# Performance work log

Hardware: AMD Instinct MI355X
Metric: run time of the kernel (lower is better)

Reference implementation:

```python
import jax, jax.numpy as jnp
import numpy as np

B, N, D, H, LH, AH = 4, 2048, 512, 4, 64, 64
NUM_BUCKETS = 128
EPS = 1e-6
LENGTHS = np.array([2048, 1536, 1024, 1792])  # jagged per-sequence lengths, sum = 6400


def _ln(x, eps=EPS):
    # F.layer_norm without affine params (biased variance)
    m = jnp.mean(x, axis=-1, keepdims=True)
    v = jnp.var(x, axis=-1, keepdims=True)
    return (x - m) * jax.lax.rsqrt(v + eps)


def _rel_bias(all_timestamps, ts_w):
    # bucketed time-delta relative attention bias -> [B, N, N]
    delta = (all_timestamps[:, :, None] - all_timestamps[:, None, :]).astype(jnp.float32)
    bucket = jnp.clip(jnp.floor(jnp.log1p(jnp.abs(delta))).astype(jnp.int32), 0, NUM_BUCKETS)
    return ts_w[bucket]


def setup_inputs() -> dict:
    key = jax.random.key(0)
    ks = jax.random.split(key, 6)
    offsets = np.concatenate([[0], np.cumsum(LENGTHS)]).astype(np.int32)
    T = int(offsets[-1])
    token_batch = np.repeat(np.arange(B), LENGTHS).astype(np.int32)
    token_pos = np.concatenate([np.arange(l) for l in LENGTHS]).astype(np.int32)
    x = jax.random.normal(ks[0], (T, D), jnp.float32)
    uvqk = jax.random.normal(ks[1], (D, 2 * LH * H + 2 * AH * H), jnp.float32) * 0.02
    o_w = jax.random.normal(ks[2], (D, LH * H), jnp.float32) * 0.02  # torch Linear weight [out, in]
    o_b = jnp.zeros((D,), jnp.float32)
    ts_w = jax.random.normal(ks[3], (NUM_BUCKETS + 1,), jnp.float32) * 0.02
    all_timestamps = jnp.sort(jax.random.randint(ks[4], (B, N), 0, 1000000, jnp.int32), axis=-1)
    invalid_attn_mask = jnp.tril(jnp.ones((N, N), jnp.float32))  # causal validity mask in {0,1}
    return {
        'x': x, 'uvqk': uvqk, 'o_w': o_w, 'o_b': o_b, 'ts_w': ts_w,
        'all_timestamps': all_timestamps, 'invalid_attn_mask': invalid_attn_mask,
        'x_offsets': jnp.asarray(offsets), 'token_batch': jnp.asarray(token_batch),
        'token_pos': jnp.asarray(token_pos),
    }


def reference(x, uvqk, o_w, o_b, ts_w, all_timestamps, invalid_attn_mask,
              x_offsets, token_batch, token_pos):
    # input layernorm + fused uvqk projection with SiLU
    h = jax.nn.silu(_ln(x) @ uvqk)  # [T, 2*H*LH + 2*H*AH]
    u, v, q, k = jnp.split(h, [LH * H, 2 * LH * H, 2 * LH * H + AH * H], axis=1)

    def pad(vals):  # jagged [T, d] -> padded dense [B, N, d]
        return jnp.zeros((B, N, vals.shape[-1]), vals.dtype).at[token_batch, token_pos].set(vals)

    pq = pad(q).reshape(B, N, H, AH)
    pk = pad(k).reshape(B, N, H, AH)
    pv = pad(v).reshape(B, N, H, LH)

    scores = jnp.einsum('bnhd,bmhd->bhnm', pq, pk)
    scores = scores + _rel_bias(all_timestamps, ts_w)[:, None]  # broadcast over heads
    scores = jax.nn.silu(scores) / N
    scores = scores * invalid_attn_mask[None, None]
    attn = jnp.einsum('bhnm,bmhd->bnhd', scores, pv).reshape(B, N, H * LH)
    attn_j = attn[token_batch, token_pos]  # dense -> jagged [T, H*LH]

    o_in = u * _ln(attn_j)
    return o_in @ o_w.T + o_b + x
```

## Files before the change

kernel.cpp:

```cpp
#include <hip/hip_runtime.h>
#include <math.h>


typedef __attribute__((ext_vector_type(8))) short bf16x8;
typedef __attribute__((ext_vector_type(4))) float f32x4;

__device__ __forceinline__ float silu_over_2048(float v) {
    return v * __builtin_amdgcn_rcpf(2048.0f + 2048.0f * __expf(-v));
}

__device__ __forceinline__ float silu_f(float v) {
    return v * __builtin_amdgcn_rcpf(1.0f + __expf(-v));
}

__device__ __forceinline__ unsigned short f2bf(float f) {
    unsigned int u = __float_as_uint(f);
    u += 0x7fffu + ((u >> 16) & 1u);
    return (unsigned short)(u >> 16);
}

__global__ __launch_bounds__(256) void k1_ln_prep(const float* __restrict__ x,
                                                  unsigned short* __restrict__ xnb,
                                                  const float* __restrict__ uvqk,
                                                  unsigned short* __restrict__ uvqkT,
                                                  const float* __restrict__ ow,
                                                  unsigned short* __restrict__ owb) {
    __shared__ float L[64][68];
    const int tid = threadIdx.x;
    const int bx = blockIdx.x;
    if (bx < 6400) {
        const float* xr = x + bx * 512;
        float a = xr[tid];
        float b = xr[tid + 256];
        float s = a + b, ss = a * a + b * b;
#pragma unroll
        for (int off = 32; off > 0; off >>= 1) {
            s += __shfl_down(s, off);
            ss += __shfl_down(ss, off);
        }
        float* red = &L[0][0];
        if ((tid & 63) == 0) { red[tid >> 6] = s; red[4 + (tid >> 6)] = ss; }
        __syncthreads();
        s = red[0] + red[1] + red[2] + red[3];
        ss = red[4] + red[5] + red[6] + red[7];
        const float mean = s * (1.0f / 512.0f);
        const float var = ss * (1.0f / 512.0f) - mean * mean;
        const float rstd = rsqrtf(var + 1e-6f);
        xnb[bx * 512 + tid] = f2bf((a - mean) * rstd);
        xnb[bx * 512 + tid + 256] = f2bf((b - mean) * rstd);
    } else if (bx < 6528) {
        const int t = bx - 6400;
        const int n0 = (t & 15) * 64;
        const int k0 = (t >> 4) * 64;
#pragma unroll
        for (int i = 0; i < 4; ++i) {
            const int r = (tid >> 4) + i * 16;
            const int c = (tid & 15) * 4;
            *(float4*)&L[r][c] = *(const float4*)(uvqk + (k0 + r) * 1024 + n0 + c);
        }
        __syncthreads();
        const int n = tid >> 2;
        const int kb = (tid & 3) * 16;
#pragma unroll
        for (int pass = 0; pass < 2; ++pass) {
            unsigned short pk[8];
#pragma unroll
            for (int j = 0; j < 8; ++j) pk[j] = f2bf(L[kb + pass * 8 + j][n]);
            *(uint4*)(uvqkT + (n0 + n) * 512 + k0 + kb + pass * 8) = *(const uint4*)pk;
        }
    } else {
        const int base = ((bx - 6528) * 256 + tid) * 8;
        float4 a = *(const float4*)(ow + base);
        float4 b = *(const float4*)(ow + base + 4);
        unsigned short pk[8] = {f2bf(a.x), f2bf(a.y), f2bf(a.z), f2bf(a.w),
                                f2bf(b.x), f2bf(b.y), f2bf(b.z), f2bf(b.w)};
        *(uint4*)(owb + base) = *(const uint4*)pk;
    }
}

__global__ __launch_bounds__(256, 4) void k2_gemm1(const unsigned short* __restrict__ A,
                                                   const unsigned short* __restrict__ Bt,
                                                   float* __restrict__ u_out,
                                                   unsigned short* __restrict__ hb,
                                                   unsigned short* __restrict__ vtb) {
    __shared__ __align__(16) unsigned short As[64][72];
    __shared__ __align__(16) unsigned short Bs[64][72];
    const int tid = threadIdx.x;
    const int lane = tid & 63;
    const int w = tid >> 6;
    const int l15 = lane & 15;
    const int quad = lane >> 4;
    const int bm = blockIdx.y * 64;
    const int bn = blockIdx.x * 64;

    f32x4 acc[4] = {};
    for (int kc = 0; kc < 512; kc += 64) {
        __syncthreads();
#pragma unroll
        for (int i = 0; i < 2; ++i) {
            const int r = (tid >> 3) + i * 32;
            const int c = (tid & 7) * 8;
            *(uint4*)&As[r][c] = *(const uint4*)(A + (bm + r) * 512 + kc + c);
            *(uint4*)&Bs[r][c] = *(const uint4*)(Bt + (bn + r) * 512 + kc + c);
        }
        __syncthreads();
        const bf16x8 a0 = *(const bf16x8*)&As[w * 16 + l15][quad * 8];
        const bf16x8 a1 = *(const bf16x8*)&As[w * 16 + l15][32 + quad * 8];
#pragma unroll
        for (int nt = 0; nt < 4; ++nt) {
            bf16x8 b0 = *(const bf16x8*)&Bs[nt * 16 + l15][quad * 8];
            bf16x8 b1 = *(const bf16x8*)&Bs[nt * 16 + l15][32 + quad * 8];
            acc[nt] = __builtin_amdgcn_mfma_f32_16x16x32_bf16(a0, b0, acc[nt], 0, 0, 0);
            acc[nt] = __builtin_amdgcn_mfma_f32_16x16x32_bf16(a1, b1, acc[nt], 0, 0, 0);
        }
    }
    const int m = bm + w * 16 + quad * 4;
    if (bn < 256) {
#pragma unroll
        for (int nt = 0; nt < 4; ++nt)
#pragma unroll
            for (int reg = 0; reg < 4; ++reg)
                u_out[(m + reg) * 256 + bn + nt * 16 + l15] = silu_f(acc[nt][reg]);
    } else if (bn < 512) {
        __syncthreads();
#pragma unroll
        for (int nt = 0; nt < 4; ++nt) {
            unsigned short pk[4];
#pragma unroll
            for (int reg = 0; reg < 4; ++reg) pk[reg] = f2bf(silu_f(acc[nt][reg]));
            *(uint2*)&As[nt * 16 + l15][w * 16 + quad * 4] = *(const uint2*)pk;
        }
        __syncthreads();
        const int sr = tid >> 3, sc = (tid & 7) * 8;
#pragma unroll
        for (int i = 0; i < 2; ++i) {
            const int r = sr + i * 32;
            *(uint4*)(vtb + (size_t)(bn - 256 + r) * 6400 + bm + sc) =
                *(const uint4*)&As[r][sc];
        }
    } else {
#pragma unroll
        for (int nt = 0; nt < 4; ++nt)
#pragma unroll
            for (int reg = 0; reg < 4; ++reg)
                hb[(m + reg) * 768 + (bn - 256) + nt * 16 + l15] = f2bf(silu_f(acc[nt][reg]));
    }
}

__global__ __launch_bounds__(256, 5) void k3_attn(const unsigned short* __restrict__ hb,
                                                  const unsigned short* __restrict__ vtb,
                                                  const int* __restrict__ ts,
                                                  const float* __restrict__ tsw,
                                                  const int* __restrict__ offs,
                                                  float* __restrict__ part) {
    const int qt = 31 - (blockIdx.x & 31);
    const int c = blockIdx.x >> 5;
    const int b = blockIdx.y;
    const int hd = blockIdx.z;
    const int off = offs[b];
    const int len = offs[b + 1] - off;
    const int nqt = len >> 6;
    if (qt >= nqt || c * 4 > qt) return;
    const int q0 = qt * 64;
    const int kt_lo = c * 4;
    const int kt_hi = min(qt, c * 4 + 3);

    __shared__ __align__(16) unsigned short QPs[64][72];
    __shared__ __align__(16) unsigned short Ks[64][72];
    __shared__ __align__(16) unsigned short Vt[64][72];
    __shared__ float tqf[64], tkf[64];
    __shared__ float tw[132];

    const int tid = threadIdx.x;
    const int lane = tid & 63;
    const int w = tid >> 6;
    const int l15 = lane & 15;
    const int quad = lane >> 4;
    const int sr = tid >> 3;
    const int sc = (tid & 7) * 8;

    if (tid < 129) tw[tid] = tsw[tid];
    if (tid < 64) tqf[tid] = (float)ts[b * 2048 + q0 + tid];
#pragma unroll
    for (int i = 0; i < 2; ++i)
        *(uint4*)&QPs[sr + i * 32][sc] =
            *(const uint4*)(hb + (off + q0 + sr + i * 32) * 768 + 256 + hd * 64 + sc);
    __syncthreads();

    const bf16x8 aQ0 = *(const bf16x8*)&QPs[w * 16 + l15][quad * 8];
    const bf16x8 aQ1 = *(const bf16x8*)&QPs[w * 16 + l15][32 + quad * 8];
    const f32x4 tq4 = *(const f32x4*)&tqf[w * 16 + quad * 4];
    const int nbase = q0 + w * 16 + quad * 4;

    f32x4 oacc[4] = {};

    for (int kt = kt_lo; kt <= kt_hi; ++kt) {
        const int m0 = kt * 64;
        __syncthreads();
#pragma unroll
        for (int i = 0; i < 2; ++i) {
            const int r = sr + i * 32;
            *(uint4*)&Ks[r][sc] =
                *(const uint4*)(hb + (off + m0 + r) * 768 + 512 + hd * 64 + sc);
            *(uint4*)&Vt[r][sc] =
                *(const uint4*)(vtb + (size_t)(hd * 64 + r) * 6400 + off + m0 + sc);
        }
        if (tid < 64) tkf[tid] = (float)ts[b * 2048 + m0 + tid];
        __syncthreads();

        f32x4 s[4] = {};
#pragma unroll
        for (int nt = 0; nt < 4; ++nt) {
            bf16x8 b0 = *(const bf16x8*)&Ks[nt * 16 + l15][quad * 8];
            bf16x8 b1 = *(const bf16x8*)&Ks[nt * 16 + l15][32 + quad * 8];
            s[nt] = __builtin_amdgcn_mfma_f32_16x16x32_bf16(aQ0, b0, s[nt], 0, 0, 0);
            s[nt] = __builtin_amdgcn_mfma_f32_16x16x32_bf16(aQ1, b1, s[nt], 0, 0, 0);
        }

        const bool diag = (kt == qt);
#pragma unroll
        for (int nt = 0; nt < 4; ++nt) {
            const int m = m0 + nt * 16 + l15;
            const float tk = tkf[nt * 16 + l15];
#pragma unroll
            for (int reg = 0; reg < 4; ++reg) {
                const float delta = fabsf(tq4[reg] - tk);
                const int bucket = (int)(__log2f(1.0f + delta) * 0.6931471805599453f);
                float val = s[nt][reg] + tw[bucket];
                float p = silu_over_2048(val);
                if (diag) p = (m <= nbase + reg) ? p : 0.0f;
                QPs[w * 16 + quad * 4 + reg][nt * 16 + l15] = f2bf(p);
            }
        }

        const bf16x8 aP0 = *(const bf16x8*)&QPs[w * 16 + l15][quad * 8];
        const bf16x8 aP1 = *(const bf16x8*)&QPs[w * 16 + l15][32 + quad * 8];
#pragma unroll
        for (int nt = 0; nt < 4; ++nt) {
            bf16x8 v0 = *(const bf16x8*)&Vt[nt * 16 + l15][quad * 8];
            bf16x8 v1 = *(const bf16x8*)&Vt[nt * 16 + l15][32 + quad * 8];
            oacc[nt] = __builtin_amdgcn_mfma_f32_16x16x32_bf16(aP0, v0, oacc[nt], 0, 0, 0);
            oacc[nt] = __builtin_amdgcn_mfma_f32_16x16x32_bf16(aP1, v1, oacc[nt], 0, 0, 0);
        }
    }

    float* pc = part + (size_t)c * (6400 * 256);
#pragma unroll
    for (int nt = 0; nt < 4; ++nt)
#pragma unroll
        for (int reg = 0; reg < 4; ++reg)
            pc[(off + q0 + w * 16 + quad * 4 + reg) * 256 + hd * 64 + nt * 16 + l15] =
                oacc[nt][reg];
}

__global__ __launch_bounds__(256) void k4a_ln(const float* __restrict__ part,
                                              const float* __restrict__ u_in,
                                              const int* __restrict__ token_pos,
                                              unsigned short* __restrict__ o_in) {
    const int row = blockIdx.x;
    const int tid = threadIdx.x;
    const int qt = token_pos[row] >> 6;
    const int nch = (qt + 4) >> 2;
    float a = 0.0f;
    for (int c = 0; c < nch; ++c) a += part[(size_t)c * (6400 * 256) + row * 256 + tid];
    float s = a, ss = a * a;
#pragma unroll
    for (int off = 32; off > 0; off >>= 1) {
        s += __shfl_down(s, off);
        ss += __shfl_down(ss, off);
    }
    __shared__ float red[8];
    if ((tid & 63) == 0) { red[tid >> 6] = s; red[4 + (tid >> 6)] = ss; }
    __syncthreads();
    s = red[0] + red[1] + red[2] + red[3];
    ss = red[4] + red[5] + red[6] + red[7];
    const float mean = s * (1.0f / 256.0f);
    const float var = ss * (1.0f / 256.0f) - mean * mean;
    const float rstd = rsqrtf(var + 1e-6f);
    const float u = u_in[row * 256 + tid];
    o_in[row * 256 + tid] = f2bf(u * (a - mean) * rstd);
}

__global__ __launch_bounds__(256, 4) void k4b_gemm2(const unsigned short* __restrict__ A,
                                                    const unsigned short* __restrict__ owb,
                                                    const float* __restrict__ ob,
                                                    const float* __restrict__ x,
                                                    float* __restrict__ out) {
    __shared__ __align__(16) unsigned short As[64][72];
    __shared__ __align__(16) unsigned short Bs[64][72];
    const int tid = threadIdx.x;
    const int lane = tid & 63;
    const int w = tid >> 6;
    const int l15 = lane & 15;
    const int quad = lane >> 4;
    const int bm = blockIdx.y * 64;
    const int bn = blockIdx.x * 64;

    f32x4 acc[4] = {};
    for (int kc = 0; kc < 256; kc += 64) {
        __syncthreads();
#pragma unroll
        for (int i = 0; i < 2; ++i) {
            const int r = (tid >> 3) + i * 32;
            const int c = (tid & 7) * 8;
            *(uint4*)&As[r][c] = *(const uint4*)(A + (bm + r) * 256 + kc + c);
            *(uint4*)&Bs[r][c] = *(const uint4*)(owb + (bn + r) * 256 + kc + c);
        }
        __syncthreads();
        const bf16x8 a0 = *(const bf16x8*)&As[w * 16 + l15][quad * 8];
        const bf16x8 a1 = *(const bf16x8*)&As[w * 16 + l15][32 + quad * 8];
#pragma unroll
        for (int nt = 0; nt < 4; ++nt) {
            bf16x8 b0 = *(const bf16x8*)&Bs[nt * 16 + l15][quad * 8];
            bf16x8 b1 = *(const bf16x8*)&Bs[nt * 16 + l15][32 + quad * 8];
            acc[nt] = __builtin_amdgcn_mfma_f32_16x16x32_bf16(a0, b0, acc[nt], 0, 0, 0);
            acc[nt] = __builtin_amdgcn_mfma_f32_16x16x32_bf16(a1, b1, acc[nt], 0, 0, 0);
        }
    }
    const int m = bm + w * 16 + quad * 4;
#pragma unroll
    for (int nt = 0; nt < 4; ++nt) {
        const int d = bn + nt * 16 + l15;
        const float bias = ob[d];
#pragma unroll
        for (int reg = 0; reg < 4; ++reg)
            out[(m + reg) * 512 + d] = acc[nt][reg] + bias + x[(m + reg) * 512 + d];
    }
}

extern "C" void kernel_launch(void* const* d_in, const int* in_sizes, int n_in,
                              void* d_out, int out_size, void* d_ws, size_t ws_size,
                              hipStream_t stream) {
    const float* x = (const float*)d_in[0];
    const float* uvqk = (const float*)d_in[1];
    const float* ow = (const float*)d_in[2];
    const float* ob = (const float*)d_in[3];
    const float* tsw = (const float*)d_in[4];
    const int* ts = (const int*)d_in[5];
    const int* offs = (const int*)d_in[7];
    const int* token_pos = (const int*)d_in[9];
    float* out = (float*)d_out;

    float* ws = (float*)d_ws;
    float* u = ws;
    float* part = u + 6400 * 256;
    unsigned short* xnb = (unsigned short*)(part + 8 * 6400 * 256);
    unsigned short* hb = xnb + 6400 * 512;
    unsigned short* o_in = hb + 6400 * 768;
    unsigned short* uvqkT = o_in + 6400 * 256;
    unsigned short* owb = uvqkT + 1024 * 512;
    unsigned short* vtb = owb + 512 * 256;

    k1_ln_prep<<<6592, 256, 0, stream>>>(x, xnb, uvqk, uvqkT, ow, owb);
    k2_gemm1<<<dim3(16, 100), 256, 0, stream>>>(xnb, uvqkT, u, hb, vtb);
    k3_attn<<<dim3(256, 4, 4), 256, 0, stream>>>(hb, vtb, ts, tsw, offs, part);
    k4a_ln<<<6400, 256, 0, stream>>>(part, u, token_pos, o_in);
    k4b_gemm2<<<dim3(8, 100), 256, 0, stream>>>(o_in, owb, ob, x, out);
}
```

Baseline: 162.7 us.

## Fuse attention-output layernorm into output projection GEMM

Merges the per-row layernorm kernel (which sums attention partials, normalises and multiplies by u) with the output-projection GEMM. Each block now covers 64 rows and 256 output columns, normalises its rows straight into LDS as bf16, and reads weights directly from global memory. This removes one kernel launch and the bf16 o_in round-trip through global memory. In exchange, the partial-sum layernorm is recomputed by both column blocks, so partial-buffer reads double, and the grid shrinks to 200 blocks, which lowers parallelism.

New measurement: 171.8 us. 1.06x slower.

```diff
diff --git a/kernel.cpp b/kernel.cpp
--- a/kernel.cpp
+++ b/kernel.cpp
@@ -253,78 +253,95 @@
                 oacc[nt][reg];
 }
 
-__global__ __launch_bounds__(256) void k4a_ln(const float* __restrict__ part,
-                                              const float* __restrict__ u_in,
-                                              const int* __restrict__ token_pos,
-                                              unsigned short* __restrict__ o_in) {
-    const int row = blockIdx.x;
+__global__ __launch_bounds__(256, 4) void k4_fused(const float* __restrict__ part,
+                                                   const float* __restrict__ u_in,
+                                                   const int* __restrict__ token_pos,
+                                                   const unsigned short* __restrict__ owb,
+                                                   const float* __restrict__ ob,
+                                                   const float* __restrict__ x,
+                                                   float* __restrict__ out) {
+    __shared__ __align__(16) unsigned short oin[64][264];
     const int tid = threadIdx.x;
-    const int qt = token_pos[row] >> 6;
-    const int nch = (qt + 4) >> 2;
-    float a = 0.0f;
-    for (int c = 0; c < nch; ++c) a += part[(size_t)c * (6400 * 256) + row * 256 + tid];
-    float s = a, ss = a * a;
-#pragma unroll
-    for (int off = 32; off > 0; off >>= 1) {
-        s += __shfl_down(s, off);
-        ss += __shfl_down(ss, off);
-    }
-    __shared__ float red[8];
-    if ((tid & 63) == 0) { red[tid >> 6] = s; red[4 + (tid >> 6)] = ss; }
+    const int bm = blockIdx.y * 64;
+    const int dn0 = blockIdx.x * 256;
+
+    {
+        const int rl = tid >> 2;
+        const int cseg = (tid & 3) * 64;
+        const int qt = token_pos[bm] >> 6;
+        const int nch = (qt + 4) >> 2;
+        f32x4 a[16] = {};
+        for (int c = 0; c < nch; ++c) {
+            const float* pr = part + (size_t)c * (6400 * 256) + (bm + rl) * 256 + cseg;
+#pragma unroll
+            for (int j = 0; j < 16; ++j) {
+                const f32x4 v = *(const f32x4*)(pr + j * 4);
+                a[j] += v;
+            }
+        }
+        float s = 0.0f, ss = 0.0f;
+#pragma unroll
+        for (int j = 0; j < 16; ++j)
+#pragma unroll
+            for (int e = 0; e < 4; ++e) { s += a[j][e]; ss += a[j][e] * a[j][e]; }
+        s += __shfl_xor(s, 1); ss += __shfl_xor(ss, 1);
+        s += __shfl_xor(s, 2); ss += __shfl_xor(ss, 2);
+        const float mean = s * (1.0f / 256.0f);
+        const float var = ss * (1.0f / 256.0f) - mean * mean;
+        const float rstd = rsqrtf(var + 1e-6f);
+        const float* ur = u_in + (bm + rl) * 256 + cseg;
+#pragma unroll
+        for (int j = 0; j < 16; j += 2) {
+            const f32x4 u0 = *(const f32x4*)(ur + j * 4);
+            const f32x4 u1 = *(const f32x4*)(ur + j * 4 + 4);
+            unsigned short pk[8];
+#pragma unroll
+            for (int e = 0; e < 4; ++e) {
+                pk[e] = f2bf(u0[e] * (a[j][e] - mean) * rstd);
+                pk[4 + e] = f2bf(u1[e] * (a[j + 1][e] - mean) * rstd);
+            }
+            *(uint4*)&oin[rl][cseg + j * 4] = *(const uint4*)pk;
+        }
+    }
     __syncthreads();
-    s = red[0] + red[1] + red[2] + red[3];
-    ss = red[4] + red[5] + red[6] + red[7];
-    const float mean = s * (1.0f / 256.0f);
-    const float var = ss * (1.0f / 256.0f) - mean * mean;
-    const float rstd = rsqrtf(var + 1e-6f);
-    const float u = u_in[row * 256 + tid];
-    o_in[row * 256 + tid] = f2bf(u * (a - mean) * rstd);
-}
-
-__global__ __launch_bounds__(256, 4) void k4b_gemm2(const unsigned short* __restrict__ A,
-                                                    const unsigned short* __restrict__ owb,
-                                                    const float* __restrict__ ob,
-                                                    const float* __restrict__ x,
-                                                    float* __restrict__ out) {
-    __shared__ __align__(16) unsigned short As[64][72];
-    __shared__ __align__(16) unsigned short Bs[64][72];
-    const int tid = threadIdx.x;
+
     const int lane = tid & 63;
     const int w = tid >> 6;
     const int l15 = lane & 15;
     const int quad = lane >> 4;
-    const int bm = blockIdx.y * 64;
-    const int bn = blockIdx.x * 64;
-
-    f32x4 acc[4] = {};
+    const int dw = dn0 + w * 64;
+
+    f32x4 acc[4][4] = {};
     for (int kc = 0; kc < 256; kc += 64) {
-        __syncthreads();
-#pragma unroll
-        for (int i = 0; i < 2; ++i) {
-            const int r = (tid >> 3) + i * 32;
-            const int c = (tid & 7) * 8;
-            *(uint4*)&As[r][c] = *(const uint4*)(A + (bm + r) * 256 + kc + c);
-            *(uint4*)&Bs[r][c] = *(const uint4*)(owb + (bn + r) * 256 + kc + c);
-        }
-        __syncthreads();
-        const bf16x8 a0 = *(const bf16x8*)&As[w * 16 + l15][quad * 8];
-        const bf16x8 a1 = *(const bf16x8*)&As[w * 16 + l15][32 + quad * 8];
-#pragma unroll
-        for (int nt = 0; nt < 4; ++nt) {
-            bf16x8 b0 = *(const bf16x8*)&Bs[nt * 16 + l15][quad * 8];
-            bf16x8 b1 = *(const bf16x8*)&Bs[nt * 16 + l15][32 + quad * 8];
-            acc[nt] = __builtin_amdgcn_mfma_f32_16x16x32_bf16(a0, b0, acc[nt], 0, 0, 0);
-            acc[nt] = __builtin_amdgcn_mfma_f32_16x16x32_bf16(a1, b1, acc[nt], 0, 0, 0);
-        }
-    }
-    const int m = bm + w * 16 + quad * 4;
+        bf16x8 aA[4][2];
+#pragma unroll
+        for (int mt = 0; mt < 4; ++mt) {
+            aA[mt][0] = *(const bf16x8*)&oin[mt * 16 + l15][kc + quad * 8];
+            aA[mt][1] = *(const bf16x8*)&oin[mt * 16 + l15][kc + 32 + quad * 8];
+        }
+#pragma unroll
+        for (int nt = 0; nt < 4; ++nt) {
+            const unsigned short* bp = owb + (dw + nt * 16 + l15) * 256 + kc;
+            const bf16x8 b0 = *(const bf16x8*)(bp + quad * 8);
+            const bf16x8 b1 = *(const bf16x8*)(bp + 32 + quad * 8);
+#pragma unroll
+            for (int mt = 0; mt < 4; ++mt) {
+                acc[mt][nt] = __builtin_amdgcn_mfma_f32_16x16x32_bf16(aA[mt][0], b0, acc[mt][nt], 0, 0, 0);
+                acc[mt][nt] = __builtin_amdgcn_mfma_f32_16x16x32_bf16(aA[mt][1], b1, acc[mt][nt], 0, 0, 0);
+            }
+        }
+    }
 #pragma unroll
     for (int nt = 0; nt < 4; ++nt) {
-        const int d = bn + nt * 16 + l15;
+        const int d = dw + nt * 16 + l15;
         const float bias = ob[d];
 #pragma unroll
-        for (int reg = 0; reg < 4; ++reg)
-            out[(m + reg) * 512 + d] = acc[nt][reg] + bias + x[(m + reg) * 512 + d];
+        for (int mt = 0; mt < 4; ++mt) {
+            const int m = bm + mt * 16 + quad * 4;
+#pragma unroll
+            for (int reg = 0; reg < 4; ++reg)
+                out[(m + reg) * 512 + d] = acc[mt][nt][reg] + bias + x[(m + reg) * 512 + d];
+        }
     }
 }
 
@@ -346,14 +363,12 @@
     float* part = u + 6400 * 256;
     unsigned short* xnb = (unsigned short*)(part + 8 * 6400 * 256);
     unsigned short* hb = xnb + 6400 * 512;
-    unsigned short* o_in = hb + 6400 * 768;
-    unsigned short* uvqkT = o_in + 6400 * 256;
+    unsigned short* uvqkT = hb + 6400 * 768;
     unsigned short* owb = uvqkT + 1024 * 512;
     unsigned short* vtb = owb + 512 * 256;
 
     k1_ln_prep<<<6592, 256, 0, stream>>>(x, xnb, uvqk, uvqkT, ow, owb);
     k2_gemm1<<<dim3(16, 100), 256, 0, stream>>>(xnb, uvqkT, u, hb, vtb);
     k3_attn<<<dim3(256, 4, 4), 256, 0, stream>>>(hb, vtb, ts, tsw, offs, part);
-    k4a_ln<<<6400, 256, 0, stream>>>(part, u, token_pos, o_in);
-    k4b_gemm2<<<dim3(8, 100), 256, 0, stream>>>(o_in, owb, ob, x, out);
-}
+    k4_fused<<<dim3(2, 100), 256, 0, stream>>>(part, u, token_pos, owb, ob, x, out);
+}
```
